# Kernel optimization log

Measured on AMD Instinct MI355X. Metric: run time of the kernel, lower is better.

## Reference

```python
import jax, jax.numpy as jnp
import numpy as np
import math

B, L, D = 2, 4096, 1024
K = D // 4


def _rotor(angles):
    # angles: [..., 6] -> scalar part s: [...], bivector part: [..., 6]
    mag = jnp.maximum(jnp.linalg.norm(angles, axis=-1), 1e-8)
    s = jnp.cos(mag)
    biv = (jnp.sin(mag) / mag)[..., None] * angles
    return s, biv


def _apply_rotor(s, biv, v):
    # s: [...], biv: [..., 6] (e12,e13,e14,e23,e24,e34), v: [..., 4]
    t12, t13, t14, t23, t24, t34 = (biv[..., i] for i in range(6))
    v1, v2, v3, v4 = (v[..., i] for i in range(4))
    s2 = s * s
    ts = 2.0 * s
    v1n = v1 * (s2 - t12 * t12 - t13 * t13 - t14 * t14) + ts * (v2 * t12 + v3 * t13 + v4 * t14)
    v2n = v2 * (s2 - t12 * t12 - t23 * t23 - t24 * t24) + ts * (-v1 * t12 + v3 * t23 + v4 * t24)
    v3n = v3 * (s2 - t13 * t13 - t23 * t23 - t34 * t34) + ts * (-v1 * t13 - v2 * t23 + v4 * t34)
    v4n = v4 * (s2 - t14 * t14 - t24 * t24 - t34 * t34) + ts * (-v1 * t14 - v2 * t24 - v3 * t34)
    return jnp.stack([v1n, v2n, v3n, v4n], axis=-1)


def _forward(x, wk1, bk1, wk2, bk2, wq1, bq1, wq2, bq2, wv, bv, ln_g, ln_b, wo, bo):
    b, l, d = x.shape
    k = d // 4
    gelu = lambda t: jax.nn.gelu(t, approximate=False)  # torch nn.GELU default = exact
    half_pi = math.pi / 2
    key_angles = (jnp.tanh(gelu(x @ wk1 + bk1) @ wk2 + bk2) * half_pi).reshape(b, l, k, 6)
    query_angles = (jnp.tanh(gelu(x @ wq1 + bq1) @ wq2 + bq2) * half_pi).reshape(b, l, k, 6)
    value = (x @ wv + bv).reshape(b, l, k, 4)
    ks, kb = _rotor(key_angles)
    qs, qb = _rotor(query_angles)
    rotated_value = _apply_rotor(ks, kb, value)          # [B,L,K,4]
    memory = jnp.cumsum(rotated_value, axis=1)            # running sum over sequence
    retrieved = _apply_rotor(qs, -qb, memory)             # reversed query rotor
    retrieved = retrieved.reshape(b, l, d)
    norm = jnp.sqrt(jnp.arange(1, l + 1, dtype=x.dtype))[None, :, None]
    r = retrieved / norm
    # LayerNorm (eps=1e-5) then Linear
    mu = jnp.mean(r, axis=-1, keepdims=True)
    var = jnp.mean((r - mu) ** 2, axis=-1, keepdims=True)
    rn = (r - mu) / jnp.sqrt(var + 1e-5) * ln_g + ln_b
    return x + rn @ wo + bo


def setup_inputs() -> dict:
    key = jax.random.key(0)
    ks = jax.random.split(key, 8)
    lin = lambda k, fi, fo: (jax.random.normal(k, (fi, fo), jnp.float32) * 0.02)
    return {
        "x": jax.random.normal(ks[0], (B, L, D), jnp.float32),
        "wk1": lin(ks[1], D, D), "bk1": jnp.zeros((D,), jnp.float32),
        "wk2": lin(ks[2], D, K * 6), "bk2": jnp.zeros((K * 6,), jnp.float32),
        "wq1": lin(ks[3], D, D), "bq1": jnp.zeros((D,), jnp.float32),
        "wq2": lin(ks[4], D, K * 6), "bq2": jnp.zeros((K * 6,), jnp.float32),
        "wv": lin(ks[5], D, D), "bv": jnp.zeros((D,), jnp.float32),
        "ln_g": jnp.ones((D,), jnp.float32), "ln_b": jnp.zeros((D,), jnp.float32),
        "wo": lin(ks[6], D, D), "bo": jnp.zeros((D,), jnp.float32),
    }


def reference(x, wk1, bk1, wk2, bk2, wq1, bq1, wq2, bq2, wv, bv, ln_g, ln_b, wo, bo):
    return _forward(x, wk1, bk1, wk2, bk2, wq1, bq1, wq2, bq2, wv, bv, ln_g, ln_b, wo, bo)
```

## Files before the change

kernel.cpp:

```cpp
#include <hip/hip_runtime.h>
#include <hip/hip_bf16.h>
#include <math.h>

#define D_DIM 1024
#define L_DIM 4096
#define B_DIM 2
#define K_DIM 256
#define N6    1536
#define M_ROWS 8192
#define CHUNKS 256
#define CHUNK_LEN 16
#define HALF_PI 1.57079632679489662f

typedef __attribute__((ext_vector_type(8))) short short8;
typedef __attribute__((ext_vector_type(4))) float f32x4;
typedef unsigned short us;

__device__ __forceinline__ void gload_lds16(const void* g, void* l) {
    __builtin_amdgcn_global_load_lds(
        (const __attribute__((address_space(1))) unsigned int*)g,
        (__attribute__((address_space(3))) unsigned int*)l,
        16, 0, 0);
}
__device__ __forceinline__ float bf2f(us u) {
    union { unsigned int i; float f; } c; c.i = ((unsigned int)u) << 16; return c.f;
}
__device__ __forceinline__ us f2bf(float v) {
    __hip_bfloat16 h = __float2bfloat16(v);
    return *(us*)&h;
}
__device__ __forceinline__ float tanh_fast(float x) {
    return 1.0f - 2.0f / (1.0f + __expf(2.0f * x));
}
__device__ __forceinline__ float gelu_exact(float v) {
    return 0.5f * v * (1.0f + erff(v * 0.70710678118654752f));
}

__device__ __forceinline__ void rotor_from_angles(const float a[6], float& s, float b[6]) {
    float m2 = a[0]*a[0] + a[1]*a[1] + a[2]*a[2] + a[3]*a[3] + a[4]*a[4] + a[5]*a[5];
    float mag = fmaxf(sqrtf(m2), 1e-8f);
    s = __cosf(mag);
    float f = __sinf(mag) / mag;
    #pragma unroll
    for (int i = 0; i < 6; ++i) b[i] = f * a[i];
}
__device__ __forceinline__ void apply_rotor(float s, const float b[6], const float v[4], float o[4]) {
    float t12 = b[0], t13 = b[1], t14 = b[2], t23 = b[3], t24 = b[4], t34 = b[5];
    float v1 = v[0], v2 = v[1], v3 = v[2], v4 = v[3];
    float s2 = s * s;
    float ts = 2.0f * s;
    o[0] = v1 * (s2 - t12*t12 - t13*t13 - t14*t14) + ts * ( v2*t12 + v3*t13 + v4*t14);
    o[1] = v2 * (s2 - t12*t12 - t23*t23 - t24*t24) + ts * (-v1*t12 + v3*t23 + v4*t24);
    o[2] = v3 * (s2 - t13*t13 - t23*t23 - t34*t34) + ts * (-v1*t13 - v2*t23 + v4*t34);
    o[3] = v4 * (s2 - t14*t14 - t24*t24 - t34*t34) + ts * (-v1*t14 - v2*t24 - v3*t34);
}

__global__ __launch_bounds__(256)
void transpose_cvt4(const float* __restrict__ w0, const float* __restrict__ w1,
                    const float* __restrict__ w2, const float* __restrict__ w3,
                    us* __restrict__ o0, us* __restrict__ o1,
                    us* __restrict__ o2, us* __restrict__ o3, int Kd, int N)
{
    const float* W = (blockIdx.z == 0) ? w0 : (blockIdx.z == 1) ? w1 : (blockIdx.z == 2) ? w2 : w3;
    us* Wt = (blockIdx.z == 0) ? o0 : (blockIdx.z == 1) ? o1 : (blockIdx.z == 2) ? o2 : o3;
    if (W == nullptr) return;
    __shared__ float sh[32][33];
    int n0 = blockIdx.x * 32, k0 = blockIdx.y * 32;
    int tx = threadIdx.x & 31, ty = threadIdx.x >> 5;
    #pragma unroll
    for (int i = 0; i < 32; i += 8)
        sh[ty + i][tx] = W[(size_t)(k0 + ty + i) * N + n0 + tx];
    __syncthreads();
    #pragma unroll
    for (int i = 0; i < 32; i += 8)
        Wt[(size_t)(n0 + ty + i) * Kd + k0 + tx] = f2bf(sh[tx][ty + i]);
}

__global__ __launch_bounds__(256)
void cvt_bf16_kernel(const float* __restrict__ in, us* __restrict__ out)
{
    size_t i = ((size_t)blockIdx.x * 256 + threadIdx.x) * 8;
    float4 v0 = *(const float4*)(in + i);
    float4 v1 = *(const float4*)(in + i + 4);
    union { us u[8]; uint4 v; } pk;
    pk.u[0] = f2bf(v0.x); pk.u[1] = f2bf(v0.y); pk.u[2] = f2bf(v0.z); pk.u[3] = f2bf(v0.w);
    pk.u[4] = f2bf(v1.x); pk.u[5] = f2bf(v1.y); pk.u[6] = f2bf(v1.z); pk.u[7] = f2bf(v1.w);
    *(uint4*)(out + i) = pk.v;
}


#define GBAR()  do { __builtin_amdgcn_s_barrier(); __builtin_amdgcn_sched_barrier(0); } while (0)

__device__ __forceinline__ void gemm128_core(
    const us* __restrict__ Ab, const us* __restrict__ Bb, int Kd,
    short* lds, f32x4 (&acc)[4][4])
{
    const int tid = threadIdx.x;
    const int l = tid & 63, w = tid >> 6;
    const int wr = w >> 1, wc = w & 1;
    const int fr = l & 15, fq = l >> 4;

    #pragma unroll
    for (int i = 0; i < 4; ++i)
        #pragma unroll
        for (int j = 0; j < 4; ++j)
            acc[i][j] = (f32x4){0.f, 0.f, 0.f, 0.f};

    const int sr = tid >> 2, su = tid & 3;
    const int slu = su ^ ((sr >> 1) & 3);
    const us* gA0 = Ab + (size_t)sr * Kd + slu * 8;
    const us* gA1 = gA0 + (size_t)64 * Kd;
    const us* gB0 = Bb + (size_t)sr * Kd + slu * 8;
    const us* gB1 = gB0 + (size_t)64 * Kd;

    const int swu = (fq ^ ((fr >> 1) & 3)) * 8;
    const int arow = (wr * 64 + fr) * 32 + swu;
    const int brow = (wc * 64 + fr) * 32 + swu;
    const int nkt = Kd >> 5;

    gload_lds16(gA0,      lds + tid * 8);
    gload_lds16(gA1,      lds + 2048 + tid * 8);
    gload_lds16(gB0,      lds + 4096 + tid * 8);
    gload_lds16(gB1,      lds + 6144 + tid * 8);
    gload_lds16(gA0 + 32, lds + 8192 + tid * 8);
    gload_lds16(gA1 + 32, lds + 8192 + 2048 + tid * 8);
    gload_lds16(gB0 + 32, lds + 8192 + 4096 + tid * 8);
    gload_lds16(gB1 + 32, lds + 8192 + 6144 + tid * 8);
    asm volatile("s_waitcnt vmcnt(4)" ::: "memory");
    GBAR();

    for (int t = 0; t < nkt; ++t) {
        const int cb = (t % 3) * 8192;
        const int sb = ((t + 2) % 3) * 8192;
        const int kp = ((t + 2) < nkt ? (t + 2) : (nkt - 1)) * 32;

        gload_lds16(gA0 + kp, lds + sb + tid * 8);
        gload_lds16(gA1 + kp, lds + sb + 2048 + tid * 8);
        gload_lds16(gB0 + kp, lds + sb + 4096 + tid * 8);
        gload_lds16(gB1 + kp, lds + sb + 6144 + tid * 8);

        short8 a[4], b[4];
        #pragma unroll
        for (int mi = 0; mi < 4; ++mi)
            a[mi] = *(const short8*)(lds + cb + arow + mi * 512);
        #pragma unroll
        for (int ni = 0; ni < 4; ++ni)
            b[ni] = *(const short8*)(lds + cb + 4096 + brow + ni * 512);

        __builtin_amdgcn_s_setprio(1);
        #pragma unroll
        for (int mi = 0; mi < 4; ++mi)
            #pragma unroll
            for (int ni = 0; ni < 4; ++ni)
                acc[mi][ni] = __builtin_amdgcn_mfma_f32_16x16x32_bf16(b[ni], a[mi], acc[mi][ni], 0, 0, 0);
        __builtin_amdgcn_sched_barrier(0);
        __builtin_amdgcn_s_setprio(0);

        asm volatile("s_waitcnt vmcnt(4)" ::: "memory");
        GBAR();
    }
}

__global__ __launch_bounds__(256, 4)
void gemm_fused3(const us* __restrict__ xb,
                 const us* __restrict__ w0t, const us* __restrict__ w1t, const us* __restrict__ w2t,
                 const float* __restrict__ b0, const float* __restrict__ b1, const float* __restrict__ b2,
                 us* __restrict__ o0, us* __restrict__ o1, us* __restrict__ o2)
{
    __shared__ short lds[24576];
    const int bm = blockIdx.x * 128;
    const int r = blockIdx.y >> 3;
    const int bn = (blockIdx.y & 7) * 128;
    const us* Bt = (r == 0) ? w0t : (r == 1) ? w1t : w2t;
    const float* bias = (r == 0) ? b0 : (r == 1) ? b1 : b2;
    us* outp = (r == 0) ? o0 : (r == 1) ? o1 : o2;
    f32x4 acc[4][4];
    gemm128_core(xb + (size_t)bm * D_DIM, Bt + (size_t)bn * D_DIM, D_DIM, lds, acc);
    const int l = threadIdx.x & 63, w = threadIdx.x >> 6;
    const int wr = w >> 1, wc = w & 1, fr = l & 15, fq = l >> 4;
    #pragma unroll
    for (int mi = 0; mi < 4; ++mi) {
        int row = bm + wr * 64 + mi * 16 + fr;
        #pragma unroll
        for (int ni = 0; ni < 4; ++ni) {
            int col = bn + wc * 64 + ni * 16 + fq * 4;
            float4 bs = *(const float4*)(bias + col);
            float v0 = acc[mi][ni][0] + bs.x, v1 = acc[mi][ni][1] + bs.y;
            float v2 = acc[mi][ni][2] + bs.z, v3 = acc[mi][ni][3] + bs.w;
            if (r < 2) { v0 = gelu_exact(v0); v1 = gelu_exact(v1); v2 = gelu_exact(v2); v3 = gelu_exact(v3); }
            ushort4 pk; pk.x = f2bf(v0); pk.y = f2bf(v1); pk.z = f2bf(v2); pk.w = f2bf(v3);
            *(ushort4*)(outp + (size_t)row * D_DIM + col) = pk;
        }
    }
}

__global__ __launch_bounds__(256, 4)
void gemm_angles(const us* __restrict__ Hk, const us* __restrict__ Hq,
                 const us* __restrict__ wk2t, const us* __restrict__ wq2t,
                 const float* __restrict__ bk2, const float* __restrict__ bq2,
                 us* __restrict__ ak, us* __restrict__ aq)
{
    __shared__ short lds[24576];
    const int z = blockIdx.z;
    const us* A  = z ? Hq : Hk;
    const us* Bt = z ? wq2t : wk2t;
    const float* bias = z ? bq2 : bk2;
    us* outp = z ? aq : ak;
    const int bm = blockIdx.x * 128;
    const int bn = blockIdx.y * 128;
    f32x4 acc[4][4];
    gemm128_core(A + (size_t)bm * D_DIM, Bt + (size_t)bn * D_DIM, D_DIM, lds, acc);
    const int l = threadIdx.x & 63, w = threadIdx.x >> 6;
    const int wr = w >> 1, wc = w & 1, fr = l & 15, fq = l >> 4;
    #pragma unroll
    for (int mi = 0; mi < 4; ++mi) {
        int row = bm + wr * 64 + mi * 16 + fr;
        #pragma unroll
        for (int ni = 0; ni < 4; ++ni) {
            int col = bn + wc * 64 + ni * 16 + fq * 4;
            float4 bs = *(const float4*)(bias + col);
            ushort4 pk;
            pk.x = f2bf(tanh_fast(acc[mi][ni][0] + bs.x) * HALF_PI);
            pk.y = f2bf(tanh_fast(acc[mi][ni][1] + bs.y) * HALF_PI);
            pk.z = f2bf(tanh_fast(acc[mi][ni][2] + bs.z) * HALF_PI);
            pk.w = f2bf(tanh_fast(acc[mi][ni][3] + bs.w) * HALF_PI);
            *(ushort4*)(outp + (size_t)row * N6 + col) = pk;
        }
    }
}

__global__ __launch_bounds__(256, 4)
void gemm_final(const us* __restrict__ rn, const us* __restrict__ wot,
                const float* __restrict__ bo, const float* __restrict__ x,
                float* __restrict__ out)
{
    __shared__ short lds[24576];
    const int bm = blockIdx.x * 128;
    const int bn = blockIdx.y * 128;
    f32x4 acc[4][4];
    gemm128_core(rn + (size_t)bm * D_DIM, wot + (size_t)bn * D_DIM, D_DIM, lds, acc);
    const int l = threadIdx.x & 63, w = threadIdx.x >> 6;
    const int wr = w >> 1, wc = w & 1, fr = l & 15, fq = l >> 4;
    #pragma unroll
    for (int mi = 0; mi < 4; ++mi) {
        int row = bm + wr * 64 + mi * 16 + fr;
        #pragma unroll
        for (int ni = 0; ni < 4; ++ni) {
            int col = bn + wc * 64 + ni * 16 + fq * 4;
            size_t off = (size_t)row * D_DIM + col;
            float4 bs = *(const float4*)(bo + col);
            float4 rx = *(const float4*)(x + off);
            float4 o;
            o.x = acc[mi][ni][0] + bs.x + rx.x;
            o.y = acc[mi][ni][1] + bs.y + rx.y;
            o.z = acc[mi][ni][2] + bs.z + rx.z;
            o.w = acc[mi][ni][3] + bs.w + rx.w;
            *(float4*)(out + off) = o;
        }
    }
}

__global__ __launch_bounds__(256)
void rot_chunk_sum(const us* __restrict__ value, const us* __restrict__ ak,
                   float4* __restrict__ sums)
{
    int bc = blockIdx.x;
    int b = bc >> 8, c = bc & 255;
    int k = threadIdx.x;
    float4 acc = make_float4(0.f, 0.f, 0.f, 0.f);
    size_t row0 = (size_t)b * L_DIM + c * CHUNK_LEN;
    for (int i = 0; i < CHUNK_LEN; ++i) {
        size_t row = row0 + i;
        ushort4 uv = *(const ushort4*)(value + row * D_DIM + k * 4);
        const unsigned int* ap = (const unsigned int*)(ak + row * N6 + k * 6);
        unsigned int a0 = ap[0], a1 = ap[1], a2 = ap[2];
        float a[6] = { bf2f(a0 & 0xffff), bf2f(a0 >> 16), bf2f(a1 & 0xffff),
                       bf2f(a1 >> 16), bf2f(a2 & 0xffff), bf2f(a2 >> 16) };
        float s, bb[6];
        rotor_from_angles(a, s, bb);
        float v[4] = {bf2f(uv.x), bf2f(uv.y), bf2f(uv.z), bf2f(uv.w)}, o[4];
        apply_rotor(s, bb, v, o);
        acc.x += o[0]; acc.y += o[1]; acc.z += o[2]; acc.w += o[3];
    }
    sums[(size_t)bc * 256 + k] = acc;
}

__global__ __launch_bounds__(256)
void scan_chunks_kernel(const float4* __restrict__ sums, float4* __restrict__ carry)
{
    int b = blockIdx.x >> 8;
    int k = blockIdx.x & 255;
    int c = threadIdx.x;
    __shared__ float4 sh[CHUNKS];
    float4 v = sums[((size_t)(b * CHUNKS + c)) * 256 + k];
    sh[c] = v;
    __syncthreads();
    for (int off = 1; off < CHUNKS; off <<= 1) {
        float4 t = make_float4(0.f, 0.f, 0.f, 0.f);
        if (c >= off) t = sh[c - off];
        __syncthreads();
        v.x += t.x; v.y += t.y; v.z += t.z; v.w += t.w;
        sh[c] = v;
        __syncthreads();
    }
    float4 ex = make_float4(0.f, 0.f, 0.f, 0.f);
    if (c > 0) ex = sh[c - 1];
    carry[((size_t)(b * CHUNKS + c)) * 256 + k] = ex;
}

__global__ __launch_bounds__(256)
void scan_apply_ln(const us* __restrict__ value, const us* __restrict__ ak,
                   const us* __restrict__ aq, const float4* __restrict__ carry,
                   const float* __restrict__ g, const float* __restrict__ bta,
                   us* __restrict__ rn)
{
    int bc = blockIdx.x;
    int b = bc >> 8, c = bc & 255;
    int k = threadIdx.x;
    int wv = k >> 6, lane = k & 63;
    float4 run = carry[(size_t)bc * 256 + k];
    float4 gv = *(const float4*)(g + k * 4);
    float4 bv = *(const float4*)(bta + k * 4);
    __shared__ float reds[4], redq[4];
    for (int i = 0; i < CHUNK_LEN; ++i) {
        int l = c * CHUNK_LEN + i;
        size_t row = (size_t)b * L_DIM + l;
        ushort4 uv = *(const ushort4*)(value + row * D_DIM + k * 4);
        const unsigned int* akp = (const unsigned int*)(ak + row * N6 + k * 6);
        unsigned int ka0 = akp[0], ka1 = akp[1], ka2 = akp[2];
        float a[6] = { bf2f(ka0 & 0xffff), bf2f(ka0 >> 16), bf2f(ka1 & 0xffff),
                       bf2f(ka1 >> 16), bf2f(ka2 & 0xffff), bf2f(ka2 >> 16) };
        float s, bb[6];
        rotor_from_angles(a, s, bb);
        float v[4] = {bf2f(uv.x), bf2f(uv.y), bf2f(uv.z), bf2f(uv.w)}, o[4];
        apply_rotor(s, bb, v, o);
        run.x += o[0]; run.y += o[1]; run.z += o[2]; run.w += o[3];
        const unsigned int* aqp = (const unsigned int*)(aq + row * N6 + k * 6);
        unsigned int qa0 = aqp[0], qa1 = aqp[1], qa2 = aqp[2];
        float aq6[6] = { bf2f(qa0 & 0xffff), bf2f(qa0 >> 16), bf2f(qa1 & 0xffff),
                         bf2f(qa1 >> 16), bf2f(qa2 & 0xffff), bf2f(qa2 >> 16) };
        float qs, qb[6];
        rotor_from_angles(aq6, qs, qb);
        #pragma unroll
        for (int t = 0; t < 6; ++t) qb[t] = -qb[t];
        float mem[4] = {run.x, run.y, run.z, run.w}, o2[4];
        apply_rotor(qs, qb, mem, o2);
        float inv = rsqrtf((float)(l + 1));
        o2[0] *= inv; o2[1] *= inv; o2[2] *= inv; o2[3] *= inv;
        float sm = o2[0] + o2[1] + o2[2] + o2[3];
        float qm = o2[0]*o2[0] + o2[1]*o2[1] + o2[2]*o2[2] + o2[3]*o2[3];
        #pragma unroll
        for (int off = 1; off < 64; off <<= 1) {
            sm += __shfl_xor(sm, off);
            qm += __shfl_xor(qm, off);
        }
        if (lane == 0) { reds[wv] = sm; redq[wv] = qm; }
        __syncthreads();
        sm = reds[0] + reds[1] + reds[2] + reds[3];
        qm = redq[0] + redq[1] + redq[2] + redq[3];
        float mu = sm * (1.0f / 1024.0f);
        float var = qm * (1.0f / 1024.0f) - mu * mu;
        float rstd = rsqrtf(var + 1e-5f);
        ushort4 pk;
        pk.x = f2bf((o2[0] - mu) * rstd * gv.x + bv.x);
        pk.y = f2bf((o2[1] - mu) * rstd * gv.y + bv.y);
        pk.z = f2bf((o2[2] - mu) * rstd * gv.z + bv.z);
        pk.w = f2bf((o2[3] - mu) * rstd * gv.w + bv.w);
        *(ushort4*)(rn + row * D_DIM + k * 4) = pk;
        __syncthreads();
    }
}

extern "C" void kernel_launch(void* const* d_in, const int* in_sizes, int n_in,
                              void* d_out, int out_size, void* d_ws, size_t ws_size,
                              hipStream_t stream)
{
    const float* x   = (const float*)d_in[0];
    const float* wk1 = (const float*)d_in[1];
    const float* bk1 = (const float*)d_in[2];
    const float* wk2 = (const float*)d_in[3];
    const float* bk2 = (const float*)d_in[4];
    const float* wq1 = (const float*)d_in[5];
    const float* bq1 = (const float*)d_in[6];
    const float* wq2 = (const float*)d_in[7];
    const float* bq2 = (const float*)d_in[8];
    const float* wv  = (const float*)d_in[9];
    const float* bv  = (const float*)d_in[10];
    const float* lng = (const float*)d_in[11];
    const float* lnb = (const float*)d_in[12];
    const float* wo  = (const float*)d_in[13];
    const float* bo  = (const float*)d_in[14];
    float* out = (float*)d_out;

    char* ws = (char*)d_ws;
    us* xb    = (us*)(ws);
    us* Hk    = (us*)(ws + (16ull  << 20));
    us* Hq    = (us*)(ws + (32ull  << 20));
    us* val   = (us*)(ws + (48ull  << 20));
    us* ak    = (us*)(ws + (64ull  << 20));
    us* aq    = (us*)(ws + (88ull  << 20));
    float4* sums  = (float4*)(ws + (112ull << 20));
    float4* carry = (float4*)(ws + (114ull << 20));
    us* wk1t  = (us*)(ws + (116ull << 20));
    us* wq1t  = (us*)(ws + (118ull << 20));
    us* wvt   = (us*)(ws + (120ull << 20));
    us* wot   = (us*)(ws + (122ull << 20));
    us* wk2t  = (us*)(ws + (124ull << 20));
    us* wq2t  = (us*)(ws + (127ull << 20));
    us* rn    = xb;

    dim3 blk(256);
    transpose_cvt4<<<dim3(D_DIM / 32, D_DIM / 32, 4), blk, 0, stream>>>(
        wk1, wq1, wv, wo, wk1t, wq1t, wvt, wot, D_DIM, D_DIM);
    transpose_cvt4<<<dim3(N6 / 32, D_DIM / 32, 2), blk, 0, stream>>>(
        wk2, wq2, nullptr, nullptr, wk2t, wq2t, nullptr, nullptr, D_DIM, N6);
    cvt_bf16_kernel<<<dim3(M_ROWS * D_DIM / (256 * 8)), blk, 0, stream>>>(x, xb);

    gemm_fused3<<<dim3(M_ROWS / 128, 24), blk, 0, stream>>>(
        xb, wk1t, wq1t, wvt, bk1, bq1, bv, Hk, Hq, val);
    gemm_angles<<<dim3(M_ROWS / 128, N6 / 128, 2), blk, 0, stream>>>(
        Hk, Hq, wk2t, wq2t, bk2, bq2, ak, aq);
    rot_chunk_sum<<<dim3(B_DIM * CHUNKS), blk, 0, stream>>>(val, ak, sums);
    scan_chunks_kernel<<<dim3(B_DIM * K_DIM), blk, 0, stream>>>(sums, carry);
    scan_apply_ln<<<dim3(B_DIM * CHUNKS), blk, 0, stream>>>(val, ak, aq, carry, lng, lnb, rn);
    gemm_final<<<dim3(M_ROWS / 128, D_DIM / 128), blk, 0, stream>>>(rn, wot, bo, x, out);
}
```

Baseline: 244.1 us.

## Prepack weights in MFMA fragment layout, load B directly to registers, swizzle XCDs

Weights are now packed into a per-fragment layout so each wave loads its B operand straight from global memory into registers, double-buffered. This removes B from LDS, halves LDS use and lowers launch bounds occupancy to 3. Grids are flattened with an XCD-aware block swizzle to improve L2 locality. Exact erf GELU is swapped for a tanh-style sigmoid approximation, which changes numerics slightly and adds some risk to accuracy.

```diff
diff --git a/kernel.cpp b/kernel.cpp
--- a/kernel.cpp
+++ b/kernel.cpp
@@ -32,8 +32,8 @@
 __device__ __forceinline__ float tanh_fast(float x) {
     return 1.0f - 2.0f / (1.0f + __expf(2.0f * x));
 }
-__device__ __forceinline__ float gelu_exact(float v) {
-    return 0.5f * v * (1.0f + erff(v * 0.70710678118654752f));
+__device__ __forceinline__ float gelu_fast(float x) {
+    return x / (1.0f + __expf(-1.5957691216057308f * x * (1.0f + 0.044715f * x * x)));
 }
 
 __device__ __forceinline__ void rotor_from_angles(const float a[6], float& s, float b[6]) {
@@ -56,24 +56,24 @@
 }
 
 __global__ __launch_bounds__(256)
-void transpose_cvt4(const float* __restrict__ w0, const float* __restrict__ w1,
-                    const float* __restrict__ w2, const float* __restrict__ w3,
-                    us* __restrict__ o0, us* __restrict__ o1,
-                    us* __restrict__ o2, us* __restrict__ o3, int Kd, int N)
+void pack_b4(const float* __restrict__ w0, const float* __restrict__ w1,
+             const float* __restrict__ w2, const float* __restrict__ w3,
+             us* __restrict__ o0, us* __restrict__ o1,
+             us* __restrict__ o2, us* __restrict__ o3, int Kd, int N)
 {
     const float* W = (blockIdx.z == 0) ? w0 : (blockIdx.z == 1) ? w1 : (blockIdx.z == 2) ? w2 : w3;
-    us* Wt = (blockIdx.z == 0) ? o0 : (blockIdx.z == 1) ? o1 : (blockIdx.z == 2) ? o2 : o3;
+    us* O = (blockIdx.z == 0) ? o0 : (blockIdx.z == 1) ? o1 : (blockIdx.z == 2) ? o2 : o3;
     if (W == nullptr) return;
-    __shared__ float sh[32][33];
-    int n0 = blockIdx.x * 32, k0 = blockIdx.y * 32;
-    int tx = threadIdx.x & 31, ty = threadIdx.x >> 5;
-    #pragma unroll
-    for (int i = 0; i < 32; i += 8)
-        sh[ty + i][tx] = W[(size_t)(k0 + ty + i) * N + n0 + tx];
-    __syncthreads();
-    #pragma unroll
-    for (int i = 0; i < 32; i += 8)
-        Wt[(size_t)(n0 + ty + i) * Kd + k0 + tx] = f2bf(sh[tx][ty + i]);
+    int nf = blockIdx.x;
+    int kt = blockIdx.y * 4 + (threadIdx.x >> 6);
+    int l = threadIdx.x & 63;
+    int n = nf * 16 + (l & 15);
+    int k0 = kt * 32 + (l >> 4) * 8;
+    union { us u[8]; uint4 v; } pk;
+    #pragma unroll
+    for (int j = 0; j < 8; ++j)
+        pk.u[j] = f2bf(W[(size_t)(k0 + j) * N + n]);
+    *(uint4*)(O + ((size_t)nf * (Kd >> 5) + kt) * 512 + l * 8) = pk.v;
 }
 
 __global__ __launch_bounds__(256)
@@ -88,94 +88,109 @@
     *(uint4*)(out + i) = pk.v;
 }
 
+__device__ __forceinline__ int xcd_swz(int bid, int nwg) {
+    int cpx = nwg >> 3;
+    return (bid & 7) * cpx + (bid >> 3);
+}
+
 
 #define GBAR()  do { __builtin_amdgcn_s_barrier(); __builtin_amdgcn_sched_barrier(0); } while (0)
 
 __device__ __forceinline__ void gemm128_core(
-    const us* __restrict__ Ab, const us* __restrict__ Bb, int Kd,
+    const us* __restrict__ Ab, const us* __restrict__ Bp, int Kd, int bn,
     short* lds, f32x4 (&acc)[4][4])
 {
     const int tid = threadIdx.x;
     const int l = tid & 63, w = tid >> 6;
     const int wr = w >> 1, wc = w & 1;
     const int fr = l & 15, fq = l >> 4;
+    const int nkt = Kd >> 5;
 
     #pragma unroll
     for (int i = 0; i < 4; ++i)
         #pragma unroll
         for (int j = 0; j < 4; ++j)
             acc[i][j] = (f32x4){0.f, 0.f, 0.f, 0.f};
+
+    const us* bptr[4];
+    #pragma unroll
+    for (int ni = 0; ni < 4; ++ni)
+        bptr[ni] = Bp + ((size_t)((bn >> 4) + wc * 4 + ni) * nkt) * 512 + l * 8;
 
     const int sr = tid >> 2, su = tid & 3;
     const int slu = su ^ ((sr >> 1) & 3);
     const us* gA0 = Ab + (size_t)sr * Kd + slu * 8;
     const us* gA1 = gA0 + (size_t)64 * Kd;
-    const us* gB0 = Bb + (size_t)sr * Kd + slu * 8;
-    const us* gB1 = gB0 + (size_t)64 * Kd;
 
     const int swu = (fq ^ ((fr >> 1) & 3)) * 8;
     const int arow = (wr * 64 + fr) * 32 + swu;
-    const int brow = (wc * 64 + fr) * 32 + swu;
-    const int nkt = Kd >> 5;
 
     gload_lds16(gA0,      lds + tid * 8);
     gload_lds16(gA1,      lds + 2048 + tid * 8);
-    gload_lds16(gB0,      lds + 4096 + tid * 8);
-    gload_lds16(gB1,      lds + 6144 + tid * 8);
-    gload_lds16(gA0 + 32, lds + 8192 + tid * 8);
-    gload_lds16(gA1 + 32, lds + 8192 + 2048 + tid * 8);
-    gload_lds16(gB0 + 32, lds + 8192 + 4096 + tid * 8);
-    gload_lds16(gB1 + 32, lds + 8192 + 6144 + tid * 8);
-    asm volatile("s_waitcnt vmcnt(4)" ::: "memory");
+    gload_lds16(gA0 + 32, lds + 4096 + tid * 8);
+    gload_lds16(gA1 + 32, lds + 6144 + tid * 8);
+    gload_lds16(gA0 + 64, lds + 8192 + tid * 8);
+    gload_lds16(gA1 + 64, lds + 10240 + tid * 8);
+    short8 bcur[4], bnxt[4];
+    #pragma unroll
+    for (int ni = 0; ni < 4; ++ni)
+        bcur[ni] = *(const short8*)(bptr[ni]);
+    asm volatile("s_waitcnt vmcnt(8)" ::: "memory");
     GBAR();
 
+    #pragma unroll 2
     for (int t = 0; t < nkt; ++t) {
-        const int cb = (t % 3) * 8192;
-        const int sb = ((t + 2) % 3) * 8192;
-        const int kp = ((t + 2) < nkt ? (t + 2) : (nkt - 1)) * 32;
-
-        gload_lds16(gA0 + kp, lds + sb + tid * 8);
-        gload_lds16(gA1 + kp, lds + sb + 2048 + tid * 8);
-        gload_lds16(gB0 + kp, lds + sb + 4096 + tid * 8);
-        gload_lds16(gB1 + kp, lds + sb + 6144 + tid * 8);
-
-        short8 a[4], b[4];
+        const int cb = (t % 3) * 4096;
+        const int sb = ((t + 2) % 3) * 4096;
+        const int ka = ((t + 2) < nkt ? (t + 2) : (nkt - 1)) * 32;
+        const int kb = ((t + 1) < nkt ? (t + 1) : (nkt - 1));
+
+        #pragma unroll
+        for (int ni = 0; ni < 4; ++ni)
+            bnxt[ni] = *(const short8*)(bptr[ni] + (size_t)kb * 512);
+        gload_lds16(gA0 + ka, lds + sb + tid * 8);
+        gload_lds16(gA1 + ka, lds + sb + 2048 + tid * 8);
+
+        short8 a[4];
         #pragma unroll
         for (int mi = 0; mi < 4; ++mi)
             a[mi] = *(const short8*)(lds + cb + arow + mi * 512);
-        #pragma unroll
-        for (int ni = 0; ni < 4; ++ni)
-            b[ni] = *(const short8*)(lds + cb + 4096 + brow + ni * 512);
 
         __builtin_amdgcn_s_setprio(1);
         #pragma unroll
         for (int mi = 0; mi < 4; ++mi)
             #pragma unroll
             for (int ni = 0; ni < 4; ++ni)
-                acc[mi][ni] = __builtin_amdgcn_mfma_f32_16x16x32_bf16(b[ni], a[mi], acc[mi][ni], 0, 0, 0);
+                acc[mi][ni] = __builtin_amdgcn_mfma_f32_16x16x32_bf16(bcur[ni], a[mi], acc[mi][ni], 0, 0, 0);
         __builtin_amdgcn_sched_barrier(0);
         __builtin_amdgcn_s_setprio(0);
 
-        asm volatile("s_waitcnt vmcnt(4)" ::: "memory");
+        #pragma unroll
+        for (int ni = 0; ni < 4; ++ni)
+            bcur[ni] = bnxt[ni];
+
+        asm volatile("s_waitcnt vmcnt(6)" ::: "memory");
         GBAR();
     }
 }
 
-__global__ __launch_bounds__(256, 4)
+__global__ __launch_bounds__(256, 3)
 void gemm_fused3(const us* __restrict__ xb,
-                 const us* __restrict__ w0t, const us* __restrict__ w1t, const us* __restrict__ w2t,
+                 const us* __restrict__ w0p, const us* __restrict__ w1p, const us* __restrict__ w2p,
                  const float* __restrict__ b0, const float* __restrict__ b1, const float* __restrict__ b2,
                  us* __restrict__ o0, us* __restrict__ o1, us* __restrict__ o2)
 {
-    __shared__ short lds[24576];
-    const int bm = blockIdx.x * 128;
-    const int r = blockIdx.y >> 3;
-    const int bn = (blockIdx.y & 7) * 128;
-    const us* Bt = (r == 0) ? w0t : (r == 1) ? w1t : w2t;
+    __shared__ short lds[12288];
+    const int wg = xcd_swz(blockIdx.x, 1536);
+    const int bm = (wg / 24) * 128;
+    const int col = wg % 24;
+    const int r = col >> 3;
+    const int bn = (col & 7) * 128;
+    const us* Bp = (r == 0) ? w0p : (r == 1) ? w1p : w2p;
     const float* bias = (r == 0) ? b0 : (r == 1) ? b1 : b2;
     us* outp = (r == 0) ? o0 : (r == 1) ? o1 : o2;
     f32x4 acc[4][4];
-    gemm128_core(xb + (size_t)bm * D_DIM, Bt + (size_t)bn * D_DIM, D_DIM, lds, acc);
+    gemm128_core(xb + (size_t)bm * D_DIM, Bp, D_DIM, bn, lds, acc);
     const int l = threadIdx.x & 63, w = threadIdx.x >> 6;
     const int wr = w >> 1, wc = w & 1, fr = l & 15, fq = l >> 4;
     #pragma unroll
@@ -183,33 +198,35 @@
         int row = bm + wr * 64 + mi * 16 + fr;
         #pragma unroll
         for (int ni = 0; ni < 4; ++ni) {
-            int col = bn + wc * 64 + ni * 16 + fq * 4;
-            float4 bs = *(const float4*)(bias + col);
+            int c0 = bn + wc * 64 + ni * 16 + fq * 4;
+            float4 bs = *(const float4*)(bias + c0);
             float v0 = acc[mi][ni][0] + bs.x, v1 = acc[mi][ni][1] + bs.y;
             float v2 = acc[mi][ni][2] + bs.z, v3 = acc[mi][ni][3] + bs.w;
-            if (r < 2) { v0 = gelu_exact(v0); v1 = gelu_exact(v1); v2 = gelu_exact(v2); v3 = gelu_exact(v3); }
+            if (r < 2) { v0 = gelu_fast(v0); v1 = gelu_fast(v1); v2 = gelu_fast(v2); v3 = gelu_fast(v3); }
             ushort4 pk; pk.x = f2bf(v0); pk.y = f2bf(v1); pk.z = f2bf(v2); pk.w = f2bf(v3);
-            *(ushort4*)(outp + (size_t)row * D_DIM + col) = pk;
+            *(ushort4*)(outp + (size_t)row * D_DIM + c0) = pk;
         }
     }
 }
 
-__global__ __launch_bounds__(256, 4)
+__global__ __launch_bounds__(256, 3)
 void gemm_angles(const us* __restrict__ Hk, const us* __restrict__ Hq,
-                 const us* __restrict__ wk2t, const us* __restrict__ wq2t,
+                 const us* __restrict__ wk2p, const us* __restrict__ wq2p,
                  const float* __restrict__ bk2, const float* __restrict__ bq2,
                  us* __restrict__ ak, us* __restrict__ aq)
 {
-    __shared__ short lds[24576];
-    const int z = blockIdx.z;
+    __shared__ short lds[12288];
+    const int wg = xcd_swz(blockIdx.x, 1536);
+    const int z = wg / 768;
+    const int rem = wg % 768;
+    const int bm = (rem / 12) * 128;
+    const int bn = (rem % 12) * 128;
     const us* A  = z ? Hq : Hk;
-    const us* Bt = z ? wq2t : wk2t;
+    const us* Bp = z ? wq2p : wk2p;
     const float* bias = z ? bq2 : bk2;
     us* outp = z ? aq : ak;
-    const int bm = blockIdx.x * 128;
-    const int bn = blockIdx.y * 128;
     f32x4 acc[4][4];
-    gemm128_core(A + (size_t)bm * D_DIM, Bt + (size_t)bn * D_DIM, D_DIM, lds, acc);
+    gemm128_core(A + (size_t)bm * D_DIM, Bp, D_DIM, bn, lds, acc);
     const int l = threadIdx.x & 63, w = threadIdx.x >> 6;
     const int wr = w >> 1, wc = w & 1, fr = l & 15, fq = l >> 4;
     #pragma unroll
@@ -217,28 +234,29 @@
         int row = bm + wr * 64 + mi * 16 + fr;
         #pragma unroll
         for (int ni = 0; ni < 4; ++ni) {
-            int col = bn + wc * 64 + ni * 16 + fq * 4;
-            float4 bs = *(const float4*)(bias + col);
+            int c0 = bn + wc * 64 + ni * 16 + fq * 4;
+            float4 bs = *(const float4*)(bias + c0);
             ushort4 pk;
             pk.x = f2bf(tanh_fast(acc[mi][ni][0] + bs.x) * HALF_PI);
             pk.y = f2bf(tanh_fast(acc[mi][ni][1] + bs.y) * HALF_PI);
             pk.z = f2bf(tanh_fast(acc[mi][ni][2] + bs.z) * HALF_PI);
             pk.w = f2bf(tanh_fast(acc[mi][ni][3] + bs.w) * HALF_PI);
-            *(ushort4*)(outp + (size_t)row * N6 + col) = pk;
+            *(ushort4*)(outp + (size_t)row * N6 + c0) = pk;
         }
     }
 }
 
-__global__ __launch_bounds__(256, 4)
-void gemm_final(const us* __restrict__ rn, const us* __restrict__ wot,
+__global__ __launch_bounds__(256, 3)
+void gemm_final(const us* __restrict__ rn, const us* __restrict__ wop,
                 const float* __restrict__ bo, const float* __restrict__ x,
                 float* __restrict__ out)
 {
-    __shared__ short lds[24576];
-    const int bm = blockIdx.x * 128;
-    const int bn = blockIdx.y * 128;
+    __shared__ short lds[12288];
+    const int wg = xcd_swz(blockIdx.x, 512);
+    const int bm = (wg / 8) * 128;
+    const int bn = (wg % 8) * 128;
     f32x4 acc[4][4];
-    gemm128_core(rn + (size_t)bm * D_DIM, wot + (size_t)bn * D_DIM, D_DIM, lds, acc);
+    gemm128_core(rn + (size_t)bm * D_DIM, wop, D_DIM, bn, lds, acc);
     const int l = threadIdx.x & 63, w = threadIdx.x >> 6;
     const int wr = w >> 1, wc = w & 1, fr = l & 15, fq = l >> 4;
     #pragma unroll
@@ -246,9 +264,9 @@
         int row = bm + wr * 64 + mi * 16 + fr;
         #pragma unroll
         for (int ni = 0; ni < 4; ++ni) {
-            int col = bn + wc * 64 + ni * 16 + fq * 4;
-            size_t off = (size_t)row * D_DIM + col;
-            float4 bs = *(const float4*)(bo + col);
+            int c0 = bn + wc * 64 + ni * 16 + fq * 4;
+            size_t off = (size_t)row * D_DIM + c0;
+            float4 bs = *(const float4*)(bo + c0);
             float4 rx = *(const float4*)(x + off);
             float4 o;
             o.x = acc[mi][ni][0] + bs.x + rx.x;
@@ -401,27 +419,27 @@
     us* aq    = (us*)(ws + (88ull  << 20));
     float4* sums  = (float4*)(ws + (112ull << 20));
     float4* carry = (float4*)(ws + (114ull << 20));
-    us* wk1t  = (us*)(ws + (116ull << 20));
-    us* wq1t  = (us*)(ws + (118ull << 20));
-    us* wvt   = (us*)(ws + (120ull << 20));
-    us* wot   = (us*)(ws + (122ull << 20));
-    us* wk2t  = (us*)(ws + (124ull << 20));
-    us* wq2t  = (us*)(ws + (127ull << 20));
+    us* wk1p  = (us*)(ws + (116ull << 20));
+    us* wq1p  = (us*)(ws + (118ull << 20));
+    us* wvp   = (us*)(ws + (120ull << 20));
+    us* wop   = (us*)(ws + (122ull << 20));
+    us* wk2p  = (us*)(ws + (124ull << 20));
+    us* wq2p  = (us*)(ws + (127ull << 20));
     us* rn    = xb;
 
     dim3 blk(256);
-    transpose_cvt4<<<dim3(D_DIM / 32, D_DIM / 32, 4), blk, 0, stream>>>(
-        wk1, wq1, wv, wo, wk1t, wq1t, wvt, wot, D_DIM, D_DIM);
-    transpose_cvt4<<<dim3(N6 / 32, D_DIM / 32, 2), blk, 0, stream>>>(
-        wk2, wq2, nullptr, nullptr, wk2t, wq2t, nullptr, nullptr, D_DIM, N6);
+    pack_b4<<<dim3(D_DIM / 16, D_DIM / 128, 4), blk, 0, stream>>>(
+        wk1, wq1, wv, wo, wk1p, wq1p, wvp, wop, D_DIM, D_DIM);
+    pack_b4<<<dim3(N6 / 16, D_DIM / 128, 2), blk, 0, stream>>>(
+        wk2, wq2, nullptr, nullptr, wk2p, wq2p, nullptr, nullptr, D_DIM, N6);
     cvt_bf16_kernel<<<dim3(M_ROWS * D_DIM / (256 * 8)), blk, 0, stream>>>(x, xb);
 
-    gemm_fused3<<<dim3(M_ROWS / 128, 24), blk, 0, stream>>>(
-        xb, wk1t, wq1t, wvt, bk1, bq1, bv, Hk, Hq, val);
-    gemm_angles<<<dim3(M_ROWS / 128, N6 / 128, 2), blk, 0, stream>>>(
-        Hk, Hq, wk2t, wq2t, bk2, bq2, ak, aq);
+    gemm_fused3<<<dim3(1536), blk, 0, stream>>>(
+        xb, wk1p, wq1p, wvp, bk1, bq1, bv, Hk, Hq, val);
+    gemm_angles<<<dim3(1536), blk, 0, stream>>>(
+        Hk, Hq, wk2p, wq2p, bk2, bq2, ak, aq);
     rot_chunk_sum<<<dim3(B_DIM * CHUNKS), blk, 0, stream>>>(val, ak, sums);
     scan_chunks_kernel<<<dim3(B_DIM * K_DIM), blk, 0, stream>>>(sums, carry);
     scan_apply_ln<<<dim3(B_DIM * CHUNKS), blk, 0, stream>>>(val, ak, aq, carry, lng, lnb, rn);
-    gemm_final<<<dim3(M_ROWS / 128, D_DIM / 128), blk, 0, stream>>>(rn, wot, bo, x, out);
-}
+    gemm_final<<<dim3(512), blk, 0, stream>>>(rn, wop, bo, x, out);
+}
```

Measured after the change: 242.6 us. Within noise of the previous version (-0.6%).
